# Performance work log

Measured on AMD Instinct MI355X. Metric: run time of the kernel, lower is better.

Reference implementation:

```python
import jax, jax.numpy as jnp
import numpy as np

HARD_RATIO = 0.5
HARD_WEIGHT = 0.5
B, Q, D = 1024, 32, 512


def _l2norm(x):
    return x / jnp.linalg.norm(x, axis=-1, keepdims=True)


def setup_inputs() -> dict:
    key = jax.random.key(0)
    k1, k2 = jax.random.split(key)
    fusion_feats = _l2norm(jax.random.normal(k1, (B, D), dtype=jnp.float32))
    target_feats = _l2norm(jax.random.normal(k2, (B, Q, D), dtype=jnp.float32))
    temp = jnp.float32(0.07)
    return {"fusion_feats": fusion_feats, "target_feats": target_feats, "temp": temp}


def reference(fusion_feats, target_feats, temp):
    b = fusion_feats.shape[0]
    # sim[i, j, q] = fusion[i] . target[j, q]  -> max over query tokens q
    sim = jnp.einsum('id,jqd->ijq', fusion_feats, target_feats)  # (B, B, Q)
    sim_max = jnp.max(sim, axis=-1) / temp                        # (B, B)

    # standard InfoNCE with diagonal labels
    loss_standard = -jnp.mean(jnp.diagonal(jax.nn.log_softmax(sim_max, axis=-1)))

    # online hard-negative mining: per-row top-k over off-diagonal entries
    num_hard = max(1, int(b * HARD_RATIO))
    diag_mask = jnp.eye(b, dtype=bool)
    masked = jnp.where(diag_mask, -jnp.inf, sim_max)
    hard_sims, _ = jax.lax.top_k(masked, num_hard)                # (B, num_hard)
    pos = jnp.diagonal(sim_max)                                    # (B,)
    # -log(exp(pos) / (exp(pos) + sum exp(hard))) = logsumexp([pos, hard]) - pos
    lse = jax.nn.logsumexp(jnp.concatenate([pos[:, None], hard_sims], axis=1), axis=1)
    hard_loss_online = jnp.mean(lse - pos)

    total_loss = loss_standard + HARD_WEIGHT * hard_loss_online
    return total_loss
```

## Files before the change

### kernel.cpp

```cpp
#include <hip/hip_runtime.h>
#include <hip/hip_bf16.h>
#include <math.h>

typedef unsigned short u16;
typedef unsigned int u32;
typedef __attribute__((ext_vector_type(4))) float f32x4;
typedef __attribute__((ext_vector_type(8))) __bf16 bf16x8;

__device__ __forceinline__ u16 f2bf(float x) {
    unsigned u = __float_as_uint(x);
    u += 0x7fffu + ((u >> 16) & 1u);
    return (u16)(u >> 16);
}
__device__ __forceinline__ unsigned pk(float lo, float hi) {
    return (unsigned)f2bf(lo) | ((unsigned)f2bf(hi) << 16);
}

__global__ void cvt_bf16(const float* __restrict__ s, u16* __restrict__ d, int n) {
    int i = (blockIdx.x * blockDim.x + threadIdx.x) * 8;
    if (i >= n) return;
    float4 v0 = *(const float4*)(s + i);
    float4 v1 = *(const float4*)(s + i + 4);
    uint4 o;
    o.x = pk(v0.x, v0.y); o.y = pk(v0.z, v0.w);
    o.z = pk(v1.x, v1.y); o.w = pk(v1.z, v1.w);
    *(uint4*)(d + i) = o;
}

#define GLB_AS __attribute__((address_space(1)))
#define LDS_AS __attribute__((address_space(3)))

__device__ __forceinline__ void gload_lds16(const void* g, void* l) {
    __builtin_amdgcn_global_load_lds((const GLB_AS void*)g, (LDS_AS void*)l, 16, 0, 0);
}

__global__ __launch_bounds__(256, 2)
void gemm_max(const u16* __restrict__ A, const u16* __restrict__ B,
              const float* __restrict__ temp_ptr, float* __restrict__ sim) {
    __shared__ __align__(16) u16 lA[128 * 32];
    __shared__ __align__(16) u16 lB[128 * 32];
    const int bn = blockIdx.x;
    const int bm = blockIdx.y;
    const int tid  = threadIdx.x;
    const int wave = tid >> 6;
    const int lane = tid & 63;
    const int wm = wave >> 1;
    const int wn = wave & 1;

    f32x4 acc[4][4] = {};

    const int rA = lane >> 2;
    const int kc = (((lane & 3) ^ ((lane >> 2) & 3)) << 3);
    const u16* gA = A + (size_t)(bm * 128 + wave * 16 + rA) * 512 + kc;
    const u16* gB = B + (size_t)(bn * 128 + wave * 16 + rA) * 512 + kc;
    u16* dA = lA + wave * 512;
    u16* dB = lB + wave * 512;

    const int frow = lane & 15;
    const int fq   = lane >> 4;
    const int fsw  = (fq ^ (frow & 3)) << 3;

    for (int k0 = 0; k0 < 512; k0 += 32) {
        gload_lds16(gA + k0,            dA);
        gload_lds16(gA + k0 + 64 * 512, dA + 2048);
        gload_lds16(gB + k0,            dB);
        gload_lds16(gB + k0 + 64 * 512, dB + 2048);
        __syncthreads();

        bf16x8 af[4], bf[4];
#pragma unroll
        for (int t = 0; t < 4; ++t) {
            af[t] = *(const bf16x8*)&lA[(wm * 64 + t * 16 + frow) * 32 + fsw];
            bf[t] = *(const bf16x8*)&lB[(wn * 64 + t * 16 + frow) * 32 + fsw];
        }
#pragma unroll
        for (int mt = 0; mt < 4; ++mt)
#pragma unroll
            for (int nt = 0; nt < 4; ++nt)
                acc[mt][nt] = __builtin_amdgcn_mfma_f32_16x16x32_bf16(
                    af[mt], bf[nt], acc[mt][nt], 0, 0, 0);
        __syncthreads();
    }

    const float tempv = *temp_ptr;
    const int quad = lane >> 4;
    const int jb = (bn * 128 + wn * 64) >> 5;
#pragma unroll
    for (int mt = 0; mt < 4; ++mt) {
#pragma unroll
        for (int rr = 0; rr < 4; ++rr) {
            float v0 = fmaxf(acc[mt][0][rr], acc[mt][1][rr]);
            float v1 = fmaxf(acc[mt][2][rr], acc[mt][3][rr]);
#pragma unroll
            for (int off = 1; off < 16; off <<= 1) {
                v0 = fmaxf(v0, __shfl_xor(v0, off));
                v1 = fmaxf(v1, __shfl_xor(v1, off));
            }
            if ((lane & 15) == 0) {
                const int row = bm * 128 + wm * 64 + mt * 16 + quad * 4 + rr;
                sim[row * 1024 + jb]     = v0 / tempv;
                sim[row * 1024 + jb + 1] = v1 / tempv;
            }
        }
    }
}

__device__ __forceinline__ u32 f2key(float x) {
    u32 b = __float_as_uint(x);
    return (b & 0x80000000u) ? ~b : (b | 0x80000000u);
}
__device__ __forceinline__ float key2f(u32 k) {
    return __uint_as_float((k & 0x80000000u) ? (k & 0x7fffffffu) : ~k);
}

__global__ __launch_bounds__(256)
void row_loss(const float* __restrict__ sim, float* __restrict__ out) {
    __shared__ u32 hist[4 * 256];
    const int tid = threadIdx.x;
    const int lane = tid & 63;
    const int wv = tid >> 6;
    const int i = blockIdx.x * 4 + wv;
    u32* h = hist + wv * 256;

    float v[16];
    const float4* rp = (const float4*)(sim + (size_t)i * 1024);
#pragma unroll
    for (int t = 0; t < 4; ++t) {
        float4 f = rp[t * 64 + lane];
        v[t * 4 + 0] = f.x; v[t * 4 + 1] = f.y; v[t * 4 + 2] = f.z; v[t * 4 + 3] = f.w;
    }

    const int dslot = ((i >> 8) << 2) | (i & 3);
    const int dlane = (i >> 2) & 63;

    u32 k[16];
#pragma unroll
    for (int t = 0; t < 16; ++t) {
        u32 kk = f2key(v[t]);
        k[t] = (lane == dlane && t == dslot) ? 0u : kk;
    }

    float pv = 0.f;
#pragma unroll
    for (int t = 0; t < 16; ++t) if (t == dslot) pv = v[t];
    const float pos = __shfl(pv, dlane);

    float m = v[0];
#pragma unroll
    for (int t = 1; t < 16; ++t) m = fmaxf(m, v[t]);
#pragma unroll
    for (int off = 32; off > 0; off >>= 1) m = fmaxf(m, __shfl_xor(m, off));
    float s = 0.f;
#pragma unroll
    for (int t = 0; t < 16; ++t) s += __expf(v[t] - m);
#pragma unroll
    for (int off = 32; off > 0; off >>= 1) s += __shfl_xor(s, off);

    const float loss_std = m + __logf(s) - pos;

    u32 prefix = 0;
    u32 r = 512;
#pragma unroll
    for (int d = 3; d >= 0; --d) {
        *(uint4*)(h + lane * 4) = uint4{0u, 0u, 0u, 0u};
        __builtin_amdgcn_wave_barrier();
#pragma unroll
        for (int t = 0; t < 16; ++t) {
            bool act = true;
            if (d < 3) act = ((k[t] >> (8 * (d + 1))) == prefix);
            if (act) atomicAdd(&h[(k[t] >> (8 * d)) & 255u], 1u);
        }
        __builtin_amdgcn_wave_barrier();
        uint4 c = *(const uint4*)(h + lane * 4);
        u32 local = c.x + c.y + c.z + c.w;
        u32 S = local;
#pragma unroll
        for (int off = 1; off < 64; off <<= 1) {
            u32 tmp = __shfl_down(S, off);
            if (lane + off < 64) S += tmp;
        }
        const u32 above = S - local;
        const u32 cg3 = above + c.w;
        const u32 cg2 = cg3 + c.z;
        const u32 cg1 = cg2 + c.y;
        const u32 cg0 = cg1 + c.x;
        int q = -1;
        if      (cg3 >= r) q = 3;
        else if (cg2 >= r) q = 2;
        else if (cg1 >= r) q = 1;
        else if (cg0 >= r) q = 0;
        int cand = (q >= 0) ? (lane * 4 + q) : -1;
#pragma unroll
        for (int off = 32; off > 0; off >>= 1) cand = max(cand, __shfl_xor(cand, off));
        const u32 cgq = (q == 3) ? cg3 : (q == 2) ? cg2 : (q == 1) ? cg1 : cg0;
        const u32 cq  = (q == 3) ? c.w : (q == 2) ? c.z : (q == 1) ? c.y : c.x;
        const u32 rp_local = r - (cgq - cq);
        r = __shfl(rp_local, cand >> 2);
        prefix = (prefix << 8) | (u32)cand;
    }

    const u32 t_key = prefix;
    const float tval = key2f(t_key);

    float se = 0.f;
    int cgt = 0;
#pragma unroll
    for (int t = 0; t < 16; ++t) {
        if (k[t] > t_key) { se += __expf(v[t] - m); ++cgt; }
    }
#pragma unroll
    for (int off = 32; off > 0; off >>= 1) se += __shfl_xor(se, off);
#pragma unroll
    for (int off = 32; off > 0; off >>= 1) cgt += __shfl_xor(cgt, off);

    const float sh = se + (float)(512 - cgt) * __expf(tval - m) + __expf(pos - m);
    const float hard = m + __logf(sh) - pos;

    if (lane == 0)
        atomicAdd(out, (loss_std + 0.5f * hard) * (1.0f / 1024.0f));
}

extern "C" void kernel_launch(void* const* d_in, const int* in_sizes, int n_in,
                              void* d_out, int out_size, void* d_ws, size_t ws_size,
                              hipStream_t stream) {
    const float* F    = (const float*)d_in[0];
    const float* T    = (const float*)d_in[1];
    const float* temp = (const float*)d_in[2];
    float* out = (float*)d_out;

    char* ws = (char*)d_ws;
    u16*  Fb  = (u16*)ws;
    u16*  Tb  = (u16*)(ws + (1u << 20));
    float* sim = (float*)(ws + (1u << 20) + (32u << 20));

    hipMemsetAsync(d_out, 0, sizeof(float), stream);

    cvt_bf16<<<256, 256, 0, stream>>>(F, Fb, 1024 * 512);
    cvt_bf16<<<8192, 256, 0, stream>>>(T, Tb, 32768 * 512);

    dim3 grid(256, 8);
    gemm_max<<<grid, 256, 0, stream>>>(Fb, Tb, temp, sim);

    row_loss<<<1024 / 4, 256, 0, stream>>>(sim, out);
}
```

Before: 173.4 us.

## Double GEMM K-tile to 64 with XOR swizzle; fuse conversions and zeroing into one kernel

The GEMM main loop now stages a 64-wide K slice per barrier pair instead of 32. This halves the number of __syncthreads and loop iterations, and it uses a new 8-way XOR swizzled LDS layout to avoid bank conflicts. The two bf16 conversion kernels and the output memset are merged into one launch to cut launch overhead. In exchange, LDS use per block doubles, which could affect occupancy, and there is still no overlap of loads with compute.

```diff
diff --git a/kernel.cpp b/kernel.cpp
--- a/kernel.cpp
+++ b/kernel.cpp
@@ -16,9 +16,16 @@
     return (unsigned)f2bf(lo) | ((unsigned)f2bf(hi) << 16);
 }
 
-__global__ void cvt_bf16(const float* __restrict__ s, u16* __restrict__ d, int n) {
-    int i = (blockIdx.x * blockDim.x + threadIdx.x) * 8;
-    if (i >= n) return;
+__global__ void cvt_fused(const float* __restrict__ F, const float* __restrict__ T,
+                          u16* __restrict__ Fb, u16* __restrict__ Tb,
+                          float* __restrict__ out) {
+    const int idx = blockIdx.x * blockDim.x + threadIdx.x;
+    if (idx == 0) out[0] = 0.f;
+    const float* s;
+    u16* d;
+    int i;
+    if (idx < 65536) { s = F; d = Fb; i = idx * 8; }
+    else             { s = T; d = Tb; i = (idx - 65536) * 8; }
     float4 v0 = *(const float4*)(s + i);
     float4 v1 = *(const float4*)(s + i + 4);
     uint4 o;
@@ -37,8 +44,8 @@
 __global__ __launch_bounds__(256, 2)
 void gemm_max(const u16* __restrict__ A, const u16* __restrict__ B,
               const float* __restrict__ temp_ptr, float* __restrict__ sim) {
-    __shared__ __align__(16) u16 lA[128 * 32];
-    __shared__ __align__(16) u16 lB[128 * 32];
+    __shared__ __align__(16) u16 lA[128 * 64];
+    __shared__ __align__(16) u16 lB[128 * 64];
     const int bn = blockIdx.x;
     const int bm = blockIdx.y;
     const int tid  = threadIdx.x;
@@ -49,41 +56,45 @@
 
     f32x4 acc[4][4] = {};
 
-    const int rA = lane >> 2;
-    const int kc = (((lane & 3) ^ ((lane >> 2) & 3)) << 3);
-    const u16* gA = A + (size_t)(bm * 128 + wave * 16 + rA) * 512 + kc;
-    const u16* gB = B + (size_t)(bn * 128 + wave * 16 + rA) * 512 + kc;
+    const int srow = lane >> 3;
+    const int skc  = ((lane & 7) ^ srow) << 3;
+    const u16* gA0 = A + (size_t)(bm * 128 + wave * 8 + srow) * 512 + skc;
+    const u16* gB0 = B + (size_t)(bn * 128 + wave * 8 + srow) * 512 + skc;
     u16* dA = lA + wave * 512;
     u16* dB = lB + wave * 512;
 
-    const int frow = lane & 15;
-    const int fq   = lane >> 4;
-    const int fsw  = (fq ^ (frow & 3)) << 3;
-
-    for (int k0 = 0; k0 < 512; k0 += 32) {
-        gload_lds16(gA + k0,            dA);
-        gload_lds16(gA + k0 + 64 * 512, dA + 2048);
-        gload_lds16(gB + k0,            dB);
-        gload_lds16(gB + k0 + 64 * 512, dB + 2048);
+    const int frow  = lane & 15;
+    const int fq    = lane >> 4;
+    const int abase = ((frow >> 3) * 512) + ((frow & 7) * 64);
+    const int c0    = (fq ^ (frow & 7)) << 3;
+
+    for (int k0 = 0; k0 < 512; k0 += 64) {
+#pragma unroll
+        for (int j = 0; j < 4; ++j) {
+            gload_lds16(gA0 + k0 + j * (32 * 512), dA + j * 2048);
+            gload_lds16(gB0 + k0 + j * (32 * 512), dB + j * 2048);
+        }
         __syncthreads();
-
-        bf16x8 af[4], bf[4];
-#pragma unroll
-        for (int t = 0; t < 4; ++t) {
-            af[t] = *(const bf16x8*)&lA[(wm * 64 + t * 16 + frow) * 32 + fsw];
-            bf[t] = *(const bf16x8*)&lB[(wn * 64 + t * 16 + frow) * 32 + fsw];
-        }
-#pragma unroll
-        for (int mt = 0; mt < 4; ++mt)
-#pragma unroll
-            for (int nt = 0; nt < 4; ++nt)
-                acc[mt][nt] = __builtin_amdgcn_mfma_f32_16x16x32_bf16(
-                    af[mt], bf[nt], acc[mt][nt], 0, 0, 0);
+#pragma unroll
+        for (int h = 0; h < 2; ++h) {
+            const int co = c0 ^ (h << 5);
+            bf16x8 af[4], bf[4];
+#pragma unroll
+            for (int t = 0; t < 4; ++t) {
+                af[t] = *(const bf16x8*)&lA[wm * 4096 + t * 1024 + abase + co];
+                bf[t] = *(const bf16x8*)&lB[wn * 4096 + t * 1024 + abase + co];
+            }
+#pragma unroll
+            for (int mt = 0; mt < 4; ++mt)
+#pragma unroll
+                for (int nt = 0; nt < 4; ++nt)
+                    acc[mt][nt] = __builtin_amdgcn_mfma_f32_16x16x32_bf16(
+                        af[mt], bf[nt], acc[mt][nt], 0, 0, 0);
+        }
         __syncthreads();
     }
 
     const float tempv = *temp_ptr;
-    const int quad = lane >> 4;
     const int jb = (bn * 128 + wn * 64) >> 5;
 #pragma unroll
     for (int mt = 0; mt < 4; ++mt) {
@@ -97,7 +108,7 @@
                 v1 = fmaxf(v1, __shfl_xor(v1, off));
             }
             if ((lane & 15) == 0) {
-                const int row = bm * 128 + wm * 64 + mt * 16 + quad * 4 + rr;
+                const int row = bm * 128 + wm * 64 + mt * 16 + fq * 4 + rr;
                 sim[row * 1024 + jb]     = v0 / tempv;
                 sim[row * 1024 + jb + 1] = v1 / tempv;
             }
@@ -233,13 +244,10 @@
     u16*  Tb  = (u16*)(ws + (1u << 20));
     float* sim = (float*)(ws + (1u << 20) + (32u << 20));
 
-    hipMemsetAsync(d_out, 0, sizeof(float), stream);
-
-    cvt_bf16<<<256, 256, 0, stream>>>(F, Fb, 1024 * 512);
-    cvt_bf16<<<8192, 256, 0, stream>>>(T, Tb, 32768 * 512);
+    cvt_fused<<<8448, 256, 0, stream>>>(F, T, Fb, Tb, out);
 
     dim3 grid(256, 8);
     gemm_max<<<grid, 256, 0, stream>>>(Fb, Tb, temp, sim);
 
-    row_loss<<<1024 / 4, 256, 0, stream>>>(sim, out);
-}
+    row_loss<<<256, 256, 0, stream>>>(sim, out);
+}
```

New measurement: 169.3 us. -2.4%, faster.
